# Optimization experiments

Measured on AMD Instinct MI355X. Metric: run time of the kernel, lower is better.

Reference implementation:

```python
import jax, jax.numpy as jnp
import numpy as np

EPS = 1e-5
B, C, N = 2, 256, 65536


def conv1x1(x, W, b):
    # Conv1d with kernel_size=1: (B,Cin,N) x (Cout,Cin) -> (B,Cout,N)
    return jnp.einsum('oc,bcn->bon', W, x) + b[None, :, None]


def instance_norm(x):
    # InstanceNorm1d, affine=False, biased variance over the spatial dim
    m = jnp.mean(x, axis=-1, keepdims=True)
    v = jnp.var(x, axis=-1, keepdims=True)
    return (x - m) * jax.lax.rsqrt(v + EPS)


def mesh_conv(x, gemm, W, b):
    # MeshCNN MeshConv: gather self + 4 one-ring neighbor edges, symmetric fns, (1,5) conv.
    Bb, Cc, E = x.shape
    xp = jnp.concatenate([jnp.zeros((Bb, Cc, 1), x.dtype), x], axis=2)  # pad slot 0 (for -1/missing)
    eid = jnp.broadcast_to(jnp.arange(E, dtype=gemm.dtype)[None, :, None], (Bb, E, 1))
    Gi = jnp.concatenate([eid, gemm], axis=2) + 1                      # (B,E,5), +1 shift for pad row
    xt = xp.transpose(0, 2, 1)                                          # (B,E+1,C)
    f = jax.vmap(lambda xb, gb: xb[gb])(xt, Gi)                         # (B,E,5,C) gather
    f = f.transpose(0, 3, 1, 2)                                         # (B,C,E,5)
    f0, f1, f2, f3, f4 = (f[..., i] for i in range(5))
    g = jnp.stack([f0, f1 + f3, f2 + f4, jnp.abs(f1 - f3), jnp.abs(f2 - f4)], axis=-1)
    # Conv2d(Cin,Cout,(1,5)) over (B,C,E,5) -> (B,Cout,E)
    return jnp.einsum('ock,bcek->boe', W, g) + b[None, :, None]


def setup_inputs() -> dict:
    key = jax.random.key(0)
    ks = jax.random.split(key, 20)
    s = 0.05
    inp = {
        'x_0': jax.random.normal(ks[0], (B, C, N), jnp.float32),
        'x_1': jax.random.normal(ks[1], (B, C, N), jnp.float32),
        'gemm': jax.random.randint(ks[2], (B, N, 4), 0, N, jnp.int32),
        # conv_a / conv_b: C -> C//4
        'Wa': jax.random.normal(ks[3], (C // 4, C), jnp.float32) * s,
        'ba': jax.random.normal(ks[4], (C // 4,), jnp.float32) * s,
        'Wb': jax.random.normal(ks[5], (C // 4, C), jnp.float32) * s,
        'bb': jax.random.normal(ks[6], (C // 4,), jnp.float32) * s,
        # conv_a_local / conv_b_local: C//2 -> C//2
        'Wal': jax.random.normal(ks[7], (C // 2, C // 2), jnp.float32) * s,
        'bal': jax.random.normal(ks[8], (C // 2,), jnp.float32) * s,
        'Wbl': jax.random.normal(ks[9], (C // 2, C // 2), jnp.float32) * s,
        'bbl': jax.random.normal(ks[10], (C // 2,), jnp.float32) * s,
        # MeshConv weights: (Cout, Cin, 5)
        'Wat': jax.random.normal(ks[11], (C // 2, C // 2, 5), jnp.float32) * s,
        'bat': jax.random.normal(ks[12], (C // 2,), jnp.float32) * s,
        'Wbt': jax.random.normal(ks[13], (C // 2, C // 2, 5), jnp.float32) * s,
        'bbt': jax.random.normal(ks[14], (C // 2,), jnp.float32) * s,
        # fuse convs: C -> C
        'Waf': jax.random.normal(ks[15], (C, C), jnp.float32) * s,
        'baf': jax.random.normal(ks[16], (C,), jnp.float32) * s,
        'Wbf': jax.random.normal(ks[17], (C, C), jnp.float32) * s,
        'bbf': jax.random.normal(ks[18], (C,), jnp.float32) * s,
    }
    return inp


def reference(x_0, x_1, gemm, Wa, ba, Wb, bb, Wal, bal, Wbl, bbl,
              Wat, bat, Wbt, bbt, Waf, baf, Wbf, bbf):
    x_a = conv1x1(x_0, Wa, ba)
    x_b = conv1x1(x_1, Wb, bb)
    x_all = jnp.concatenate([x_a, x_b], axis=1)          # (B, C/2, N)
    a_local = conv1x1(x_all, Wal, bal)
    a_tri = mesh_conv(x_all, gemm, Wat, bat)
    x_a_two = jnp.concatenate([a_local, a_tri], axis=1)  # (B, C, N)
    b_local = conv1x1(x_all, Wbl, bbl)
    b_tri = mesh_conv(x_all, gemm, Wbt, bbt)
    x_b_two = jnp.concatenate([b_local, b_tri], axis=1)
    wa = jax.nn.sigmoid(instance_norm(conv1x1(x_a_two, Waf, baf)))
    wb = jax.nn.sigmoid(instance_norm(conv1x1(x_b_two, Wbf, bbf)))
    w = jax.nn.softmax(jnp.stack([wa, wb], axis=1), axis=1)  # (B,2,C,N)
    return x_0 * w[:, 0] + x_1 * w[:, 1]
```

## Files before the change

### kernel.cpp

```cpp
#include <hip/hip_runtime.h>
#include <stdint.h>

#define NEDGE 65536

typedef __attribute__((ext_vector_type(4))) float f32x4;
typedef __attribute__((ext_vector_type(8))) __bf16 bf16x8;

#define VMCNT(n) asm volatile("s_waitcnt vmcnt(" #n ")" ::: "memory")
#define LGKM0 asm volatile("s_waitcnt lgkmcnt(0)" ::: "memory")
#define SCHEDB __builtin_amdgcn_sched_barrier(0)

__device__ __forceinline__ uint16_t f2bf(float f) {
  union { float f; uint32_t u; } v; v.f = f;
  uint32_t r = v.u + 0x7FFFu + ((v.u >> 16) & 1u);
  return (uint16_t)(r >> 16);
}
__device__ __forceinline__ float bflo(uint32_t u) {
  union { uint32_t u; float f; } v; v.u = u << 16; return v.f;
}
__device__ __forceinline__ float bfhi(uint32_t u) {
  union { uint32_t u; float f; } v; v.u = u & 0xFFFF0000u; return v.f;
}
__device__ __forceinline__ uint32_t packbf(float lo, float hi) {
  return (uint32_t)f2bf(lo) | ((uint32_t)f2bf(hi) << 16);
}
__device__ __forceinline__ void gload_lds16(const void* g, void* l) {
  __builtin_amdgcn_global_load_lds(
      (__attribute__((address_space(1))) uint32_t*)(uintptr_t)g,
      (__attribute__((address_space(3))) uint32_t*)l, 16, 0, 0);
}
__device__ __forceinline__ float sigm(float z) { return 1.0f / (1.0f + __expf(-z)); }

__global__ void k_compose(const float* __restrict__ Wal, const float* __restrict__ Wbl,
                          const float* __restrict__ Wat, const float* __restrict__ Wbt,
                          const float* __restrict__ Waf, const float* __restrict__ Wbf,
                          uint16_t* __restrict__ Wt) {
  int id = blockIdx.x * 256 + threadIdx.x;
  if (id >= 512 * 640) return;
  int j = id / 640, kk = id % 640;
  const float* Wf = (j < 256) ? Waf : Wbf;
  const float* Wl = (j < 256) ? Wal : Wbl;
  const float* Wr = (j < 256) ? Wat : Wbt;
  int jj = j & 255;
  float acc = 0.f;
  if (kk < 128) {
    int c = kk;
    for (int o = 0; o < 128; ++o) acc += Wl[o * 128 + c] * Wf[jj * 256 + o];
    for (int o = 0; o < 128; ++o) acc += Wr[(o * 128 + c) * 5 + 0] * Wf[jj * 256 + 128 + o];
  } else {
    int blkid = (kk - 128) >> 7;
    int gk = (blkid == 0) ? 1 : (blkid == 1) ? 3 : (blkid == 2) ? 2 : 4;
    int c = (kk - 128) & 127;
    for (int o = 0; o < 128; ++o) acc += Wr[(o * 128 + c) * 5 + gk] * Wf[jj * 256 + 128 + o];
  }
  Wt[j * 640 + kk] = f2bf(acc);
}

__global__ void k_bias(const float* __restrict__ bal, const float* __restrict__ bat,
                       const float* __restrict__ baf, const float* __restrict__ bbl,
                       const float* __restrict__ bbt, const float* __restrict__ bbf,
                       const float* __restrict__ Waf, const float* __restrict__ Wbf,
                       float* __restrict__ biasF) {
  int id = blockIdx.x * 256 + threadIdx.x;
  if (id >= 512) return;
  const float* Wf = (id < 256) ? Waf : Wbf;
  const float* bl = (id < 256) ? bal : bbl;
  const float* bt = (id < 256) ? bat : bbt;
  const float* bsf = (id < 256) ? baf : bbf;
  int jj = id & 255;
  float acc = bsf[jj];
  for (int o = 0; o < 128; ++o) acc += Wf[jj * 256 + o] * bl[o];
  for (int o = 0; o < 128; ++o) acc += Wf[jj * 256 + 128 + o] * bt[o];
  biasF[id] = acc;
}

__global__ void k_wt1(const float* __restrict__ Wa, const float* __restrict__ Wb,
                      uint16_t* __restrict__ W1bf) {
  int id = blockIdx.x * 256 + threadIdx.x;
  if (id >= 2 * 64 * 256) return;
  int side = id >> 14, r = id & 16383;
  W1bf[id] = f2bf(side ? Wb[r] : Wa[r]);
}

__global__ __launch_bounds__(256) void k1_xa(
    const float* __restrict__ x0, const float* __restrict__ x1,
    const uint16_t* __restrict__ W1bf, const float* __restrict__ ba,
    const float* __restrict__ bb, uint16_t* __restrict__ XA) {
  __shared__ __align__(16) float Xs[3][32 * 128];
  __shared__ __align__(16) uint16_t Bs[64 * 256];
  int t = threadIdx.x;
  int L = blockIdx.x;
  int xcd = L & 7, jj = L >> 3;
  int ntile = xcd * 64 + (jj & 63);
  int sideb = jj >> 6;
  int side = sideb & 1, b = sideb >> 1;
  int n0 = ntile * 128;
  const float* xin = (side ? x1 : x0) + (size_t)b * 256 * NEDGE + n0;
  const uint16_t* wsrc = W1bf + side * 64 * 256;

#pragma unroll
  for (int q = 0; q < 8; ++q) {
    int s = q * 256 + t;
    int j = s >> 5, pb = s & 31;
    int lb = pb ^ (j & 7);
    gload_lds16(wsrc + j * 256 + lb * 8, &Bs[s * 8]);
  }
#pragma unroll
  for (int c = 0; c < 2; ++c) {
#pragma unroll
    for (int q = 0; q < 4; ++q) {
      int s = q * 256 + t;
      int cl = s >> 5, pb = s & 31;
      int lb = pb ^ (((cl >> 3) & 3) << 2);
      gload_lds16(xin + (size_t)(c * 32 + cl) * NEDGE + lb * 4, &Xs[c][s * 4]);
    }
  }

  int wv = t >> 6, l = t & 63;
  int m = l & 15, g = l >> 4;
  int pcol[2];
#pragma unroll
  for (int nf = 0; nf < 2; ++nf) {
    int n = wv * 32 + nf * 16 + m;
    pcol[nf] = (((n >> 2) ^ (g << 2)) << 2) + (n & 3);
  }

  f32x4 acc[2][4];
  f32x4 zero = {0.f, 0.f, 0.f, 0.f};
#pragma unroll
  for (int nf = 0; nf < 2; ++nf)
#pragma unroll
    for (int jf = 0; jf < 4; ++jf) acc[nf][jf] = zero;

#pragma unroll
  for (int ks = 0; ks < 8; ++ks) {
    if (ks < 6) {
      const float* xc = xin + (size_t)(ks + 2) * 32 * NEDGE;
#pragma unroll
      for (int q = 0; q < 4; ++q) {
        int s = q * 256 + t;
        int cl = s >> 5, pb = s & 31;
        int lb = pb ^ (((cl >> 3) & 3) << 2);
        gload_lds16(xc + (size_t)cl * NEDGE + lb * 4, &Xs[(ks + 2) % 3][s * 4]);
      }
      VMCNT(8);
    } else if (ks == 6) {
      VMCNT(4);
    } else {
      VMCNT(0);
    }
    SCHEDB;
    __builtin_amdgcn_s_barrier();
    SCHEDB;

    const float* Xb = Xs[ks % 3];
    bf16x8 af[4];
#pragma unroll
    for (int jf = 0; jf < 4; ++jf) {
      int jloc = jf * 16 + m;
      int pbb = (ks * 4 + g) ^ (jloc & 7);
      af[jf] = *(const bf16x8*)&Bs[jloc * 256 + pbb * 8];
    }
#pragma unroll
    for (int nf = 0; nf < 2; ++nf) {
      const float* base = Xb + g * 8 * 128 + pcol[nf];
      float xv[8];
#pragma unroll
      for (int i = 0; i < 8; ++i) xv[i] = base[i * 128];
      union { bf16x8 v; uint32_t u[4]; } bx;
      bx.u[0] = packbf(xv[0], xv[1]);
      bx.u[1] = packbf(xv[2], xv[3]);
      bx.u[2] = packbf(xv[4], xv[5]);
      bx.u[3] = packbf(xv[6], xv[7]);
#pragma unroll
      for (int jf = 0; jf < 4; ++jf)
        acc[nf][jf] = __builtin_amdgcn_mfma_f32_16x16x32_bf16(af[jf], bx.v, acc[nf][jf], 0, 0, 0);
    }
    LGKM0;
    __builtin_amdgcn_s_barrier();
    SCHEDB;
  }

  const float* bias = side ? bb : ba;
  uint16_t* XAb = XA + (size_t)b * NEDGE * 128;
#pragma unroll
  for (int jf = 0; jf < 4; ++jf) {
    f32x4 bv = *(const f32x4*)(bias + jf * 16 + g * 4);
#pragma unroll
    for (int nf = 0; nf < 2; ++nf) {
      int n = n0 + wv * 32 + nf * 16 + m;
      uint2 o;
      o.x = packbf(acc[nf][jf][0] + bv[0], acc[nf][jf][1] + bv[1]);
      o.y = packbf(acc[nf][jf][2] + bv[2], acc[nf][jf][3] + bv[3]);
      *(uint2*)(XAb + (size_t)n * 128 + side * 64 + jf * 16 + g * 4) = o;
    }
  }
}

__global__ __launch_bounds__(512, 2) void k23_gemm(
    const uint16_t* __restrict__ XAb, const int* __restrict__ gidx,
    const uint16_t* __restrict__ Wt, const float* __restrict__ biasF,
    uint16_t* __restrict__ Y, float* __restrict__ part) {
  __shared__ __align__(16) uint16_t As[2][128 * 64];
  __shared__ __align__(16) uint16_t Bs[256 * 64];
  __shared__ int gi[512];
  __shared__ float sL[2][256][2];
  int t = threadIdx.x;
  int L = blockIdx.x;
  int xcd = L & 7, jz = L >> 3;
  int bx = xcd * 64 + (jz >> 1);
  int jbase = (jz & 1) * 256;
  int ebase = bx * 128;
  int wid = t >> 6, lane = t & 63;
  int wr = wid >> 2, wc = wid & 3;
  int m = lane & 15, g = lane >> 4;

  gi[t] = gidx[(size_t)ebase * 4 + t];

#define ISSUE_BS(s_)                                                            \
  do {                                                                          \
    _Pragma("unroll")                                                           \
    for (int q = 0; q < 4; ++q) {                                               \
      int slot = q * 512 + t; int r = slot >> 3, c16 = slot & 7;                \
      gload_lds16(Wt + (size_t)(jbase + r) * 640 + (s_) * 64 + (c16 ^ (r & 7)) * 8, \
                  &Bs[slot * 8]);                                               \
    }                                                                           \
  } while (0)

#pragma unroll
  for (int s = 0; s < 2; ++s) {
#pragma unroll
    for (int q = 0; q < 2; ++q) {
      int slot = q * 512 + t;
      int r = slot >> 3, c16 = slot & 7;
      gload_lds16(XAb + (size_t)(ebase + r) * 128 + s * 64 + (c16 ^ (r & 7)) * 8,
                  &As[s][slot * 8]);
    }
  }
  ISSUE_BS(0);
  __syncthreads();

  const int r0 = t >> 3, cc = t & 7;
  int iP13[2], iQ13[2], iP24[2], iQ24[2];
#pragma unroll
  for (int q2 = 0; q2 < 2; ++q2) {
    int r = r0 + q2 * 64;
    iP13[q2] = gi[r * 4 + 0]; iQ13[q2] = gi[r * 4 + 2];
    iP24[q2] = gi[r * 4 + 1]; iQ24[q2] = gi[r * 4 + 3];
  }

  uint4 grP[2], grQ[2];
#define ISSUE_GATH(v)                                                           \
  do {                                                                          \
    const int coffv = ((v) & 1) * 64;                                           \
    const int pr = ((v) - 2) >> 2;                                              \
    _Pragma("unroll")                                                           \
    for (int q2 = 0; q2 < 2; ++q2) {                                            \
      int ip = pr ? iP24[q2] : iP13[q2];                                        \
      int iq = pr ? iQ24[q2] : iQ13[q2];                                        \
      grP[q2] = *(const uint4*)(XAb + (size_t)ip * 128 + coffv + cc * 8);       \
      grQ[q2] = *(const uint4*)(XAb + (size_t)iq * 128 + coffv + cc * 8);       \
    }                                                                           \
  } while (0)

  ISSUE_GATH(2);

  f32x4 acc[4][4];
  f32x4 zero = {0.f, 0.f, 0.f, 0.f};
#pragma unroll
  for (int r = 0; r < 4; ++r)
#pragma unroll
    for (int c = 0; c < 4; ++c) acc[r][c] = zero;

#pragma unroll
  for (int u = 0; u < 10; ++u) {
    if (u >= 1) ISSUE_BS(u);
    if (u >= 1 && u <= 8) {
      VMCNT(4);
      SCHEDB;
      const int su = u + 1;
      const bool sum_op = (((su - 2) >> 1) & 1) == 0;
#pragma unroll
      for (int q2 = 0; q2 < 2; ++q2) {
        int r = r0 + q2 * 64;
        uint4 P = grP[q2], Q = grQ[q2];
        uint4 R;
        if (sum_op) {
          R.x = packbf(bflo(P.x) + bflo(Q.x), bfhi(P.x) + bfhi(Q.x));
          R.y = packbf(bflo(P.y) + bflo(Q.y), bfhi(P.y) + bfhi(Q.y));
          R.z = packbf(bflo(P.z) + bflo(Q.z), bfhi(P.z) + bfhi(Q.z));
          R.w = packbf(bflo(P.w) + bflo(Q.w), bfhi(P.w) + bfhi(Q.w));
        } else {
          R.x = packbf(fabsf(bflo(P.x) - bflo(Q.x)), fabsf(bfhi(P.x) - bfhi(Q.x)));
          R.y = packbf(fabsf(bflo(P.y) - bflo(Q.y)), fabsf(bfhi(P.y) - bfhi(Q.y)));
          R.z = packbf(fabsf(bflo(P.z) - bflo(Q.z)), fabsf(bfhi(P.z) - bfhi(Q.z)));
          R.w = packbf(fabsf(bflo(P.w) - bflo(Q.w)), fabsf(bfhi(P.w) - bfhi(Q.w)));
        }
        *(uint4*)&As[su & 1][(r * 8 + (cc ^ (r & 7))) * 8] = R;
      }
    }
    if (u >= 1 && u <= 7) ISSUE_GATH(u + 2);
    if (u <= 7) { VMCNT(4); } else { VMCNT(0); }
    LGKM0;
    SCHEDB;
    __builtin_amdgcn_s_barrier();
    SCHEDB;

    const uint16_t* Ab = As[u & 1];
#pragma unroll
    for (int kit = 0; kit < 2; ++kit) {
      bf16x8 af[4], bf[4];
#pragma unroll
      for (int r = 0; r < 4; ++r) {
        int row = wr * 64 + r * 16 + m;
        af[r] = *(const bf16x8*)&Ab[row * 64 + ((kit * 4 + g) ^ (m & 7)) * 8];
      }
#pragma unroll
      for (int cf = 0; cf < 4; ++cf) {
        int row = wc * 64 + cf * 16 + m;
        bf[cf] = *(const bf16x8*)&Bs[row * 64 + ((kit * 4 + g) ^ (m & 7)) * 8];
      }
#pragma unroll
      for (int r = 0; r < 4; ++r)
#pragma unroll
        for (int cf = 0; cf < 4; ++cf)
          acc[r][cf] = __builtin_amdgcn_mfma_f32_16x16x32_bf16(bf[cf], af[r], acc[r][cf], 0, 0, 0);
    }
    __builtin_amdgcn_s_barrier();
    SCHEDB;
  }
#undef ISSUE_GATH
#undef ISSUE_BS

  float s1[4][4], s2[4][4];
#pragma unroll
  for (int cf = 0; cf < 4; ++cf)
#pragma unroll
    for (int q = 0; q < 4; ++q) { s1[cf][q] = 0.f; s2[cf][q] = 0.f; }

#pragma unroll
  for (int cf = 0; cf < 4; ++cf) {
    f32x4 bv = *(const f32x4*)(biasF + jbase + wc * 64 + cf * 16 + g * 4);
#pragma unroll
    for (int r = 0; r < 4; ++r) {
      int eg = ebase + wr * 64 + r * 16 + m;
      float v0 = acc[r][cf][0] + bv[0];
      float v1 = acc[r][cf][1] + bv[1];
      float v2 = acc[r][cf][2] + bv[2];
      float v3 = acc[r][cf][3] + bv[3];
      s1[cf][0] += v0; s2[cf][0] += v0 * v0;
      s1[cf][1] += v1; s2[cf][1] += v1 * v1;
      s1[cf][2] += v2; s2[cf][2] += v2 * v2;
      s1[cf][3] += v3; s2[cf][3] += v3 * v3;
      uint2 o;
      o.x = packbf(v0, v1);
      o.y = packbf(v2, v3);
      *(uint2*)(Y + (size_t)eg * 512 + jbase + wc * 64 + cf * 16 + g * 4) = o;
    }
  }
#pragma unroll
  for (int cf = 0; cf < 4; ++cf)
#pragma unroll
    for (int q = 0; q < 4; ++q) {
#pragma unroll
      for (int off = 1; off < 16; off <<= 1) {
        s1[cf][q] += __shfl_xor(s1[cf][q], off);
        s2[cf][q] += __shfl_xor(s2[cf][q], off);
      }
    }
  if (m == 0) {
#pragma unroll
    for (int cf = 0; cf < 4; ++cf)
#pragma unroll
      for (int q = 0; q < 4; ++q) {
        int jl = wc * 64 + cf * 16 + g * 4 + q;
        sL[wr][jl][0] = s1[cf][q];
        sL[wr][jl][1] = s2[cf][q];
      }
  }
  __syncthreads();
  if (t < 256) {
    float a1 = sL[0][t][0] + sL[1][t][0];
    float a2 = sL[0][t][1] + sL[1][t][1];
    float* p = part + ((size_t)bx * 512 + jbase + t) * 2;
    p[0] = a1; p[1] = a2;
  }
}

__global__ void k3b2(const float* __restrict__ part, float* __restrict__ statF) {
  int col = blockIdx.x, t = threadIdx.x;
  float s1 = 0, s2 = 0;
  for (int k = t; k < 512; k += 128) {
    const float* p = part + ((size_t)k * 512 + col) * 2;
    s1 += p[0]; s2 += p[1];
  }
  for (int off = 32; off; off >>= 1) { s1 += __shfl_down(s1, off); s2 += __shfl_down(s2, off); }
  __shared__ float sh[4];
  if ((t & 63) == 0) { sh[(t >> 6) * 2] = s1; sh[(t >> 6) * 2 + 1] = s2; }
  __syncthreads();
  if (t == 0) {
    s1 = sh[0] + sh[2]; s2 = sh[1] + sh[3];
    float mean = s1 * (1.0f / 65536.0f);
    float var = s2 * (1.0f / 65536.0f) - mean * mean;
    statF[col * 2] = mean;
    statF[col * 2 + 1] = rsqrtf(var + 1e-5f);
  }
}

__global__ __launch_bounds__(256) void k4_final(
    const uint16_t* __restrict__ Y, const float* __restrict__ statF,
    const float* __restrict__ x0b, const float* __restrict__ x1b,
    float* __restrict__ outb) {
  __shared__ float W0[128][65];
  __shared__ float mA[128], rA[128], mB[128], rB[128];
  int t = threadIdx.x;
  int L = blockIdx.x;
  int xcd = L & 7, jz = L >> 3;
  int n0 = (xcd * 128 + (jz >> 1)) * 64;
  int ch = jz & 1;
  if (t < 128) {
    mA[t] = statF[(ch * 128 + t) * 2];
    rA[t] = statF[(ch * 128 + t) * 2 + 1];
  } else {
    int q = t - 128;
    mB[q] = statF[(256 + ch * 128 + q) * 2];
    rB[q] = statF[(256 + ch * 128 + q) * 2 + 1];
  }
  __syncthreads();
  const char* Ybase = (const char*)Y;
  for (int i = t; i < 64 * 64; i += 256) {
    int row = i >> 6, cp = i & 63;
    const char* yr = Ybase + (size_t)(n0 + row) * 1024;
    uint32_t ya2 = *(const uint32_t*)(yr + ch * 256 + cp * 4);
    uint32_t yb2 = *(const uint32_t*)(yr + 512 + ch * 256 + cp * 4);
    int c0 = 2 * cp, c1 = 2 * cp + 1;
    float wa0 = sigm((bflo(ya2) - mA[c0]) * rA[c0]);
    float wa1 = sigm((bfhi(ya2) - mA[c1]) * rA[c1]);
    float wb0 = sigm((bflo(yb2) - mB[c0]) * rB[c0]);
    float wb1 = sigm((bfhi(yb2) - mB[c1]) * rB[c1]);
    W0[c0][row] = sigm(wa0 - wb0);
    W0[c1][row] = sigm(wa1 - wb1);
  }
  __syncthreads();
  int nn = t & 63, cg = t >> 6;
  for (int cc2 = cg; cc2 < 128; cc2 += 4) {
    int c = ch * 128 + cc2;
    size_t gidx2 = (size_t)c * NEDGE + n0 + nn;
    float w0 = W0[cc2][nn];
    outb[gidx2] = x0b[gidx2] * w0 + x1b[gidx2] * (1.0f - w0);
  }
}

extern "C" void kernel_launch(void* const* d_in, const int* in_sizes, int n_in,
                              void* d_out, int out_size, void* d_ws, size_t ws_size,
                              hipStream_t stream) {
  const float* x0 = (const float*)d_in[0];
  const float* x1 = (const float*)d_in[1];
  const int* gemm = (const int*)d_in[2];
  const float* Wa = (const float*)d_in[3];
  const float* ba = (const float*)d_in[4];
  const float* Wb = (const float*)d_in[5];
  const float* bb = (const float*)d_in[6];
  const float* Wal = (const float*)d_in[7];
  const float* bal = (const float*)d_in[8];
  const float* Wbl = (const float*)d_in[9];
  const float* bbl = (const float*)d_in[10];
  const float* Wat = (const float*)d_in[11];
  const float* bat = (const float*)d_in[12];
  const float* Wbt = (const float*)d_in[13];
  const float* bbt = (const float*)d_in[14];
  const float* Waf = (const float*)d_in[15];
  const float* baf = (const float*)d_in[16];
  const float* Wbf = (const float*)d_in[17];
  const float* bbf = (const float*)d_in[18];
  float* out = (float*)d_out;

  char* ws = (char*)d_ws;
  uint16_t* XA   = (uint16_t*)ws;
  uint16_t* Yb   = (uint16_t*)(ws + 33554432);
  uint16_t* Wt   = (uint16_t*)(ws + 100663296);
  uint16_t* W1bf = (uint16_t*)(ws + 101318656);
  float*    biasF= (float*)(ws + 101384192);
  float*    part = (float*)(ws + 101386240);
  float*    statF= (float*)(ws + 103483392);

  k_compose<<<dim3(1280), dim3(256), 0, stream>>>(Wal, Wbl, Wat, Wbt, Waf, Wbf, Wt);
  k_bias<<<dim3(2), dim3(256), 0, stream>>>(bal, bat, baf, bbl, bbt, bbf, Waf, Wbf, biasF);
  k_wt1<<<dim3(128), dim3(256), 0, stream>>>(Wa, Wb, W1bf);
  k1_xa<<<dim3(2048), dim3(256), 0, stream>>>(x0, x1, W1bf, ba, bb, XA);

  for (int b = 0; b < 2; ++b) {
    const uint16_t* XAb = XA + (size_t)b * NEDGE * 128;
    k23_gemm<<<dim3(1024), dim3(512), 0, stream>>>(
        XAb, gemm + (size_t)b * NEDGE * 4, Wt, biasF, Yb, part);
    k3b2<<<dim3(512), dim3(128), 0, stream>>>(part, statF + b * 1024);
    k4_final<<<dim3(2048), dim3(256), 0, stream>>>(
        Yb, statF + b * 1024, x0 + (size_t)b * 256 * NEDGE,
        x1 + (size_t)b * 256 * NEDGE, out + (size_t)b * 256 * NEDGE);
  }
}
```

Measured before the change: 419.9 us.

## Halve K-step to 32 and double-buffer weights to deepen gemm pipeline

```diff
diff --git a/kernel.cpp b/kernel.cpp
--- a/kernel.cpp
+++ b/kernel.cpp
@@ -197,14 +197,13 @@
   }
 }
 
-__global__ __launch_bounds__(512, 2) void k23_gemm(
+__global__ __launch_bounds__(512) void k23_gemm(
     const uint16_t* __restrict__ XAb, const int* __restrict__ gidx,
     const uint16_t* __restrict__ Wt, const float* __restrict__ biasF,
     uint16_t* __restrict__ Y, float* __restrict__ part) {
-  __shared__ __align__(16) uint16_t As[2][128 * 64];
-  __shared__ __align__(16) uint16_t Bs[256 * 64];
+  __shared__ __align__(16) uint16_t As[2][128 * 32];
+  __shared__ __align__(16) uint16_t Bs[2][256 * 32];
   __shared__ int gi[512];
-  __shared__ float sL[2][256][2];
   int t = threadIdx.x;
   int L = blockIdx.x;
   int xcd = L & 7, jz = L >> 3;
@@ -216,28 +215,6 @@
   int m = lane & 15, g = lane >> 4;
 
   gi[t] = gidx[(size_t)ebase * 4 + t];
-
-#define ISSUE_BS(s_)                                                            \
-  do {                                                                          \
-    _Pragma("unroll")                                                           \
-    for (int q = 0; q < 4; ++q) {                                               \
-      int slot = q * 512 + t; int r = slot >> 3, c16 = slot & 7;                \
-      gload_lds16(Wt + (size_t)(jbase + r) * 640 + (s_) * 64 + (c16 ^ (r & 7)) * 8, \
-                  &Bs[slot * 8]);                                               \
-    }                                                                           \
-  } while (0)
-
-#pragma unroll
-  for (int s = 0; s < 2; ++s) {
-#pragma unroll
-    for (int q = 0; q < 2; ++q) {
-      int slot = q * 512 + t;
-      int r = slot >> 3, c16 = slot & 7;
-      gload_lds16(XAb + (size_t)(ebase + r) * 128 + s * 64 + (c16 ^ (r & 7)) * 8,
-                  &As[s][slot * 8]);
-    }
-  }
-  ISSUE_BS(0);
   __syncthreads();
 
   const int r0 = t >> 3, cc = t & 7;
@@ -249,21 +226,69 @@
     iP24[q2] = gi[r * 4 + 1]; iQ24[q2] = gi[r * 4 + 3];
   }
 
-  uint4 grP[2], grQ[2];
-#define ISSUE_GATH(v)                                                           \
+  uint4 grP[2][2], grQ[2][2];
+
+#define ISSUE_ASD(u_)                                                           \
   do {                                                                          \
-    const int coffv = ((v) & 1) * 64;                                           \
-    const int pr = ((v) - 2) >> 2;                                              \
+    int r = t >> 2, cb = t & 3;                                                 \
+    gload_lds16(XAb + (size_t)(ebase + r) * 128 + (u_) * 32 + ((cb ^ (r & 3)) * 8), \
+                &As[(u_) & 1][t * 8]);                                          \
+  } while (0)
+
+#define ISSUE_BSC(u_)                                                           \
+  do {                                                                          \
+    _Pragma("unroll")                                                           \
+    for (int q = 0; q < 2; ++q) {                                               \
+      int s = q * 512 + t; int r = s >> 2, cb = s & 3;                          \
+      gload_lds16(Wt + (size_t)(jbase + r) * 640 + (u_) * 32 + ((cb ^ (r & 3)) * 8), \
+                  &Bs[(u_) & 1][s * 8]);                                        \
+    }                                                                           \
+  } while (0)
+
+#define ISSUE_G(v_)                                                             \
+  do {                                                                          \
+    const int coffv = ((v_) & 1) * 64;                                          \
+    const int pr = ((v_) - 2) >> 2;                                             \
+    const int bk = (v_) & 1;                                                    \
     _Pragma("unroll")                                                           \
     for (int q2 = 0; q2 < 2; ++q2) {                                            \
       int ip = pr ? iP24[q2] : iP13[q2];                                        \
       int iq = pr ? iQ24[q2] : iQ13[q2];                                        \
-      grP[q2] = *(const uint4*)(XAb + (size_t)ip * 128 + coffv + cc * 8);       \
-      grQ[q2] = *(const uint4*)(XAb + (size_t)iq * 128 + coffv + cc * 8);       \
+      grP[bk][q2] = *(const uint4*)(XAb + (size_t)ip * 128 + coffv + cc * 8);   \
+      grQ[bk][q2] = *(const uint4*)(XAb + (size_t)iq * 128 + coffv + cc * 8);   \
     }                                                                           \
   } while (0)
 
-  ISSUE_GATH(2);
+#define FEAT(v_, h_, u_)                                                        \
+  do {                                                                          \
+    if ((cc >> 2) == (h_)) {                                                    \
+      const int bk = (v_) & 1;                                                  \
+      const bool sum_op = ((((v_) - 2) >> 1) & 1) == 0;                         \
+      _Pragma("unroll")                                                         \
+      for (int q2 = 0; q2 < 2; ++q2) {                                          \
+        int r = r0 + q2 * 64;                                                   \
+        uint4 P = grP[bk][q2], Q = grQ[bk][q2];                                 \
+        uint4 R;                                                                \
+        if (sum_op) {                                                           \
+          R.x = packbf(bflo(P.x) + bflo(Q.x), bfhi(P.x) + bfhi(Q.x));           \
+          R.y = packbf(bflo(P.y) + bflo(Q.y), bfhi(P.y) + bfhi(Q.y));           \
+          R.z = packbf(bflo(P.z) + bflo(Q.z), bfhi(P.z) + bfhi(Q.z));           \
+          R.w = packbf(bflo(P.w) + bflo(Q.w), bfhi(P.w) + bfhi(Q.w));           \
+        } else {                                                                \
+          R.x = packbf(fabsf(bflo(P.x) - bflo(Q.x)), fabsf(bfhi(P.x) - bfhi(Q.x))); \
+          R.y = packbf(fabsf(bflo(P.y) - bflo(Q.y)), fabsf(bfhi(P.y) - bfhi(Q.y))); \
+          R.z = packbf(fabsf(bflo(P.z) - bflo(Q.z)), fabsf(bfhi(P.z) - bfhi(Q.z))); \
+          R.w = packbf(fabsf(bflo(P.w) - bflo(Q.w)), fabsf(bfhi(P.w) - bfhi(Q.w))); \
+        }                                                                       \
+        *(uint4*)&As[(u_) & 1][(r * 4 + ((cc & 3) ^ (r & 3))) * 8] = R;         \
+      }                                                                         \
+    }                                                                           \
+  } while (0)
+
+  ISSUE_ASD(0);
+  ISSUE_BSC(0);
+  ISSUE_ASD(1);
+  ISSUE_BSC(1);
 
   f32x4 acc[4][4];
   f32x4 zero = {0.f, 0.f, 0.f, 0.f};
@@ -273,64 +298,69 @@
     for (int c = 0; c < 4; ++c) acc[r][c] = zero;
 
 #pragma unroll
-  for (int u = 0; u < 10; ++u) {
-    if (u >= 1) ISSUE_BS(u);
-    if (u >= 1 && u <= 8) {
-      VMCNT(4);
+  for (int u = 0; u < 20; ++u) {
+    if (u == 0) {
+      VMCNT(3);
+    } else if (u == 1) {
+      ISSUE_ASD(2); ISSUE_BSC(2);
+      VMCNT(3);
+    } else if (u == 2) {
+      ISSUE_ASD(3); ISSUE_BSC(3); ISSUE_G(2);
+      VMCNT(7);
+    } else if (u == 3) {
+      ISSUE_BSC(4);
+      VMCNT(6);
+    } else if (u <= 17 && (u & 1) == 0) {
+      VMCNT(2);
       SCHEDB;
-      const int su = u + 1;
-      const bool sum_op = (((su - 2) >> 1) & 1) == 0;
-#pragma unroll
-      for (int q2 = 0; q2 < 2; ++q2) {
-        int r = r0 + q2 * 64;
-        uint4 P = grP[q2], Q = grQ[q2];
-        uint4 R;
-        if (sum_op) {
-          R.x = packbf(bflo(P.x) + bflo(Q.x), bfhi(P.x) + bfhi(Q.x));
-          R.y = packbf(bflo(P.y) + bflo(Q.y), bfhi(P.y) + bfhi(Q.y));
-          R.z = packbf(bflo(P.z) + bflo(Q.z), bfhi(P.z) + bfhi(Q.z));
-          R.w = packbf(bflo(P.w) + bflo(Q.w), bfhi(P.w) + bfhi(Q.w));
-        } else {
-          R.x = packbf(fabsf(bflo(P.x) - bflo(Q.x)), fabsf(bfhi(P.x) - bfhi(Q.x)));
-          R.y = packbf(fabsf(bflo(P.y) - bflo(Q.y)), fabsf(bfhi(P.y) - bfhi(Q.y)));
-          R.z = packbf(fabsf(bflo(P.z) - bflo(Q.z)), fabsf(bfhi(P.z) - bfhi(Q.z)));
-          R.w = packbf(fabsf(bflo(P.w) - bflo(Q.w)), fabsf(bfhi(P.w) - bfhi(Q.w)));
-        }
-        *(uint4*)&As[su & 1][(r * 8 + (cc ^ (r & 7))) * 8] = R;
-      }
-    }
-    if (u >= 1 && u <= 7) ISSUE_GATH(u + 2);
-    if (u <= 7) { VMCNT(4); } else { VMCNT(0); }
+      FEAT(u >> 1, 0, u);
+      ISSUE_BSC(u + 1);
+      ISSUE_G((u >> 1) + 1);
+      VMCNT(6);
+    } else if (u <= 17) {
+      FEAT(u >> 1, 1, u);
+      ISSUE_BSC(u + 1);
+      VMCNT(6);
+    } else if (u == 18) {
+      VMCNT(2);
+      SCHEDB;
+      FEAT(9, 0, 18);
+      ISSUE_BSC(19);
+      VMCNT(2);
+    } else {
+      FEAT(9, 1, 19);
+      VMCNT(0);
+    }
     LGKM0;
     SCHEDB;
     __builtin_amdgcn_s_barrier();
     SCHEDB;
 
     const uint16_t* Ab = As[u & 1];
-#pragma unroll
-    for (int kit = 0; kit < 2; ++kit) {
-      bf16x8 af[4], bf[4];
-#pragma unroll
-      for (int r = 0; r < 4; ++r) {
-        int row = wr * 64 + r * 16 + m;
-        af[r] = *(const bf16x8*)&Ab[row * 64 + ((kit * 4 + g) ^ (m & 7)) * 8];
-      }
-#pragma unroll
-      for (int cf = 0; cf < 4; ++cf) {
-        int row = wc * 64 + cf * 16 + m;
-        bf[cf] = *(const bf16x8*)&Bs[row * 64 + ((kit * 4 + g) ^ (m & 7)) * 8];
-      }
-#pragma unroll
-      for (int r = 0; r < 4; ++r)
-#pragma unroll
-        for (int cf = 0; cf < 4; ++cf)
-          acc[r][cf] = __builtin_amdgcn_mfma_f32_16x16x32_bf16(bf[cf], af[r], acc[r][cf], 0, 0, 0);
-    }
+    const uint16_t* Bb = Bs[u & 1];
+    bf16x8 af[4], bf[4];
+#pragma unroll
+    for (int r = 0; r < 4; ++r) {
+      int row = wr * 64 + r * 16 + m;
+      af[r] = *(const bf16x8*)&Ab[(row * 4 + (g ^ (m & 3))) * 8];
+    }
+#pragma unroll
+    for (int cf = 0; cf < 4; ++cf) {
+      int row = wc * 64 + cf * 16 + m;
+      bf[cf] = *(const bf16x8*)&Bb[(row * 4 + (g ^ (m & 3))) * 8];
+    }
+#pragma unroll
+    for (int r = 0; r < 4; ++r)
+#pragma unroll
+      for (int cf = 0; cf < 4; ++cf)
+        acc[r][cf] = __builtin_amdgcn_mfma_f32_16x16x32_bf16(bf[cf], af[r], acc[r][cf], 0, 0, 0);
     __builtin_amdgcn_s_barrier();
     SCHEDB;
   }
-#undef ISSUE_GATH
-#undef ISSUE_BS
+#undef ISSUE_ASD
+#undef ISSUE_BSC
+#undef ISSUE_G
+#undef FEAT
 
   float s1[4][4], s2[4][4];
 #pragma unroll
@@ -374,23 +404,17 @@
 #pragma unroll
       for (int q = 0; q < 4; ++q) {
         int jl = wc * 64 + cf * 16 + g * 4 + q;
-        sL[wr][jl][0] = s1[cf][q];
-        sL[wr][jl][1] = s2[cf][q];
+        float* p = part + (((size_t)bx * 2 + wr) * 512 + jbase + jl) * 2;
+        p[0] = s1[cf][q];
+        p[1] = s2[cf][q];
       }
-  }
-  __syncthreads();
-  if (t < 256) {
-    float a1 = sL[0][t][0] + sL[1][t][0];
-    float a2 = sL[0][t][1] + sL[1][t][1];
-    float* p = part + ((size_t)bx * 512 + jbase + t) * 2;
-    p[0] = a1; p[1] = a2;
   }
 }
 
 __global__ void k3b2(const float* __restrict__ part, float* __restrict__ statF) {
   int col = blockIdx.x, t = threadIdx.x;
   float s1 = 0, s2 = 0;
-  for (int k = t; k < 512; k += 128) {
+  for (int k = t; k < 1024; k += 128) {
     const float* p = part + ((size_t)k * 512 + col) * 2;
     s1 += p[0]; s2 += p[1];
   }
@@ -482,7 +506,7 @@
   uint16_t* W1bf = (uint16_t*)(ws + 101318656);
   float*    biasF= (float*)(ws + 101384192);
   float*    part = (float*)(ws + 101386240);
-  float*    statF= (float*)(ws + 103483392);
+  float*    statF= (float*)(ws + 105580544);
 
   k_compose<<<dim3(1280), dim3(256), 0, stream>>>(Wal, Wbl, Wat, Wbt, Waf, Wbf, Wt);
   k_bias<<<dim3(2), dim3(256), 0, stream>>>(bal, bat, baf, bbl, bbt, bbf, Waf, Wbf, biasF);
```

New measurement: 572.8 us. +36.4%, slower.
